# Kernel optimization log

Hardware: AMD Instinct MI355X
Metric: run time of the kernel (lower is better)

Reference implementation:

```python
import jax, jax.numpy as jnp
import numpy as np

B, S, D, H, FF = 4, 1024, 1024, 16, 4096
DH = D // H
EPS = 1e-5  # torch LayerNorm default


def _layernorm(x, g, b):
    m = jnp.mean(x, axis=-1, keepdims=True)
    v = jnp.mean((x - m) ** 2, axis=-1, keepdims=True)
    return (x - m) * jax.lax.rsqrt(v + EPS) * g + b


def setup_inputs() -> dict:
    key = jax.random.key(0)
    ks = jax.random.split(key, 8)
    init = lambda k, shape: jax.random.normal(k, shape, jnp.float32) * 0.02
    return {
        "x": jax.random.normal(ks[0], (B, S, D), jnp.float32),
        "Wq": init(ks[1], (D, D)), "bq": jnp.zeros((D,), jnp.float32),
        "Wk": init(ks[2], (D, D)), "bk": jnp.zeros((D,), jnp.float32),
        "Wv": init(ks[3], (D, D)), "bv": jnp.zeros((D,), jnp.float32),
        "Wo": init(ks[4], (D, D)), "bo": jnp.zeros((D,), jnp.float32),
        "ln1_g": jnp.ones((D,), jnp.float32), "ln1_b": jnp.zeros((D,), jnp.float32),
        "W1": init(ks[5], (D, FF)), "b1": jnp.zeros((FF,), jnp.float32),
        "W2": init(ks[6], (FF, D)), "b2": jnp.zeros((D,), jnp.float32),
        "ln2_g": jnp.ones((D,), jnp.float32), "ln2_b": jnp.zeros((D,), jnp.float32),
    }


def reference(x, Wq, bq, Wk, bk, Wv, bv, Wo, bo,
              ln1_g, ln1_b, W1, b1, W2, b2, ln2_g, ln2_b):
    Bx, Sx, _ = x.shape

    def heads(w, b):  # [B,S,D] -> [B,H,S,DH]
        return (x @ w + b).reshape(Bx, Sx, H, DH).transpose(0, 2, 1, 3)

    q, k, v = heads(Wq, bq), heads(Wk, bk), heads(Wv, bv)
    scores = jnp.einsum('bhqd,bhkd->bhqk', q, k) / jnp.sqrt(jnp.float32(DH))
    causal = jnp.tril(jnp.ones((Sx, Sx), bool))
    scores = jnp.where(causal[None, None], scores, jnp.float32(-1e9))
    attn = jax.nn.softmax(scores, axis=-1)           # [B,H,S,S]
    ctx = jnp.einsum('bhqk,bhkd->bqhd', attn, v).reshape(Bx, Sx, D)
    attn_out = ctx @ Wo + bo
    h = _layernorm(x + attn_out, ln1_g, ln1_b)
    ff = jax.nn.relu(h @ W1 + b1) @ W2 + b2
    y = _layernorm(h + ff, ln2_g, ln2_b)
    return (y, attn)
```

## Files before the change

kernel.cpp:

```cpp
#include <hip/hip_runtime.h>
#include <cstdint>


#define T_B 4
#define T_S 1024
#define T_D 1024
#define T_H 16
#define T_DH 64
#define T_FF 4096
#define T_TOK (T_B * T_S)

typedef __attribute__((ext_vector_type(8))) short bf16x8;
typedef __attribute__((ext_vector_type(4))) float f32x4;

__device__ __forceinline__ short f2bf(float f) {
  uint32_t u = __float_as_uint(f);
  u += 0x7FFFu + ((u >> 16) & 1u);
  return (short)(u >> 16);
}

__device__ __forceinline__ float bf2f(short s) {
  return __uint_as_float(((uint32_t)(unsigned short)s) << 16);
}

__device__ __forceinline__ void async_copy16(void* lds, const void* g) {
  __builtin_amdgcn_global_load_lds(
      (__attribute__((address_space(1))) uint32_t*)(uintptr_t)g,
      (__attribute__((address_space(3))) uint32_t*)(uint32_t)(uintptr_t)lds,
      16, 0, 0);
}

__device__ __forceinline__ void stage32(short* dstA, short* dstB,
                                        const short* A, int lda, const short* Bm,
                                        int ldb, int m0, int n0, int k0, int t,
                                        int wid) {
  const int row0 = t >> 2;
  const int cb0 = (t & 3) << 4;
  async_copy16((char*)dstA + (wid << 10),
               (const char*)A + (((size_t)(m0 + row0) * lda + k0) << 1) + cb0);
  async_copy16((char*)dstA + 4096 + (wid << 10),
               (const char*)A + (((size_t)(m0 + 64 + row0) * lda + k0) << 1) + cb0);
  async_copy16((char*)dstB + (wid << 10),
               (const char*)Bm + (((size_t)(n0 + row0) * ldb + k0) << 1) + cb0);
  async_copy16((char*)dstB + 4096 + (wid << 10),
               (const char*)Bm + (((size_t)(n0 + 64 + row0) * ldb + k0) << 1) + cb0);
}

__device__ __forceinline__ void compute32(const short* As, const short* Bs,
                                          int wm, int wn, int quad, int r16,
                                          f32x4 acc[4][4]) {
  bf16x8 av[4], bv[4];
#pragma unroll
  for (int i = 0; i < 4; ++i) {
    av[i] = *(const bf16x8*)(As + ((wm + i * 16 + r16) << 5) + (quad << 3));
    bv[i] = *(const bf16x8*)(Bs + ((wn + i * 16 + r16) << 5) + (quad << 3));
  }
#pragma unroll
  for (int mi = 0; mi < 4; ++mi)
#pragma unroll
    for (int ni = 0; ni < 4; ++ni)
      acc[mi][ni] = __builtin_amdgcn_mfma_f32_16x16x32_bf16(av[mi], bv[ni],
                                                            acc[mi][ni], 0, 0, 0);
}

__device__ __forceinline__ void mfma_loop_bk64(
    const short* __restrict__ A, int lda, const short* __restrict__ Bm, int ldb,
    int kLen, int m0, int n0, short* As, short* As2, short* Bs, short* Bs2,
    f32x4 acc[4][4]) {
  const int t = threadIdx.x;
  const int lane = t & 63, wid = t >> 6;
  const int wm = (wid >> 1) << 6, wn = (wid & 1) << 6;
  const int quad = lane >> 4, r16 = lane & 15;
  const f32x4 zf = {0.f, 0.f, 0.f, 0.f};
#pragma unroll
  for (int i = 0; i < 4; ++i)
#pragma unroll
    for (int j = 0; j < 4; ++j) acc[i][j] = zf;
  for (int k0 = 0; k0 < kLen; k0 += 64) {
    __syncthreads();
    stage32(As, Bs, A, lda, Bm, ldb, m0, n0, k0, t, wid);
    stage32(As2, Bs2, A, lda, Bm, ldb, m0, n0, k0 + 32, t, wid);
    __syncthreads();
    compute32(As, Bs, wm, wn, quad, r16, acc);
    compute32(As2, Bs2, wm, wn, quad, r16, acc);
  }
}

template <int MODE>
__global__ __launch_bounds__(256) void gemm_dense(
    const short* __restrict__ A, const short* __restrict__ Bw, int K, int N,
    const float* __restrict__ bias0, const float* __restrict__ bias1,
    const float* __restrict__ bias2, short* __restrict__ outb0,
    short* __restrict__ outb1, short* __restrict__ outb2) {
  __shared__ __align__(16) char smem[MODE == 0 ? 34816 : 32768];
  short* As = (short*)smem;
  short* As2 = As + 4096;
  short* Bs = As + 8192;
  short* Bs2 = As + 12288;
  const int m0 = blockIdx.x << 7, n0 = blockIdx.y << 7;
  f32x4 acc[4][4];
  mfma_loop_bk64(A, K, Bw, K, K, m0, n0, As, As2, Bs, Bs2, acc);

  const int t = threadIdx.x;
  const int lane = t & 63, wid = t >> 6;
  const int wm = (wid >> 1) << 6, wn = (wid & 1) << 6;
  const int quad = lane >> 4, r16 = lane & 15;

  if constexpr (MODE == 0) {
    const int which = n0 >> 10;
    const float* bias = (which == 0) ? bias0 : (which == 1) ? bias1 : bias2;
    if (which < 2) {
      short* outp = (which == 0) ? outb0 : outb1;
#pragma unroll
      for (int mi = 0; mi < 4; ++mi) {
#pragma unroll
        for (int ni = 0; ni < 4; ++ni) {
          const int col = n0 + wn + ni * 16 + r16;
          const int c10 = col & 1023;
          const float bb = bias[c10];
          const int hh = c10 >> 6, dh = col & 63;
#pragma unroll
          for (int reg = 0; reg < 4; ++reg) {
            const int row = m0 + wm + mi * 16 + quad * 4 + reg;
            const int b = row >> 10, s = row & 1023;
            outp[((((size_t)b * T_H + hh) * T_S) + s) * T_DH + dh] =
                f2bf(acc[mi][ni][reg] + bb);
          }
        }
      }
    } else {
      __syncthreads();
      short* vtile = (short*)smem;
#pragma unroll
      for (int mi = 0; mi < 4; ++mi)
#pragma unroll
        for (int ni = 0; ni < 4; ++ni) {
          const int c = wn + ni * 16 + r16;
          const float bb = bias[(n0 + c) & 1023];
#pragma unroll
          for (int reg = 0; reg < 4; ++reg) {
            const int r = wm + mi * 16 + quad * 4 + reg;
            vtile[c * 136 + r] = f2bf(acc[mi][ni][reg] + bb);
          }
        }
      __syncthreads();
      const int b = m0 >> 10, s0 = m0 & 1023;
      const int c = t >> 1, half = t & 1;
      const int c10 = (n0 + c) & 1023;
      const int hh = c10 >> 6, dh = c10 & 63;
      short* dst = outb2 + (((size_t)b * T_H + hh) * T_DH + dh) * T_S + s0 + half * 64;
      const short* srcl = vtile + c * 136 + half * 64;
#pragma unroll
      for (int j = 0; j < 8; ++j)
        *(bf16x8*)(dst + j * 8) = *(const bf16x8*)(srcl + j * 8);
    }
  } else {
#pragma unroll
    for (int mi = 0; mi < 4; ++mi)
#pragma unroll
      for (int ni = 0; ni < 4; ++ni) {
        const int col = n0 + wn + ni * 16 + r16;
        const float bb = bias0[col];
#pragma unroll
        for (int reg = 0; reg < 4; ++reg) {
          const int row = m0 + wm + mi * 16 + quad * 4 + reg;
          outb0[(size_t)row * N + col] = f2bf(fmaxf(acc[mi][ni][reg] + bb, 0.f));
        }
      }
  }
}

__global__ __launch_bounds__(256) void gemm_splitk(
    const short* __restrict__ A, const short* __restrict__ Bw, int K, int N,
    int kc, float* __restrict__ outp) {
  __shared__ __align__(16) char smem[32768];
  short* As = (short*)smem;
  short* As2 = As + 4096;
  short* Bs = As + 8192;
  short* Bs2 = As + 12288;
  const int m0 = blockIdx.x << 7, n0 = blockIdx.y << 7, z = blockIdx.z;
  f32x4 acc[4][4];
  mfma_loop_bk64(A + (size_t)z * kc, K, Bw + (size_t)z * kc, K, kc, m0, n0, As,
                 As2, Bs, Bs2, acc);
  float* o = outp + (size_t)z * T_TOK * N;
  const int t = threadIdx.x;
  const int lane = t & 63, wid = t >> 6;
  const int wm = (wid >> 1) << 6, wn = (wid & 1) << 6;
  const int quad = lane >> 4, r16 = lane & 15;
#pragma unroll
  for (int mi = 0; mi < 4; ++mi)
#pragma unroll
    for (int ni = 0; ni < 4; ++ni) {
      const int col = n0 + wn + ni * 16 + r16;
#pragma unroll
      for (int reg = 0; reg < 4; ++reg) {
        const int row = m0 + wm + mi * 16 + quad * 4 + reg;
        o[(size_t)row * N + col] = acc[mi][ni][reg];
      }
    }
}

__global__ __launch_bounds__(256) void attn_pass1(
    const short* __restrict__ qg, const short* __restrict__ kg,
    const short* __restrict__ vg, short* __restrict__ ctx,
    float* __restrict__ rsinv_g) {
  const int qb = blockIdx.x;
  const int bh = blockIdx.y;
  const int b = bh >> 4, h = bh & 15;
  const int m0 = qb << 7;
  __shared__ __align__(16) short Es[4 * 128 * 32];
  __shared__ float rsbuf[2][128];
  const int t = threadIdx.x;
  const int lane = t & 63, wid = t >> 6;
  const int quad = lane >> 4, r16 = lane & 15;
  const int wm = (wid >> 1) << 6, wn = (wid & 1) << 6;
  const int pvm = wid << 5;

  const short* Qbh = qg + (size_t)bh * T_S * T_DH;
  const short* Kbh = kg + (size_t)bh * T_S * T_DH;
  const short* Vbh = vg + (size_t)bh * T_DH * T_S;

  bf16x8 qf[4][2];
#pragma unroll
  for (int mi = 0; mi < 4; ++mi)
#pragma unroll
    for (int ksd = 0; ksd < 2; ++ksd)
      qf[mi][ksd] = *(const bf16x8*)(Qbh + (size_t)(m0 + wm + mi * 16 + r16) * T_DH +
                                     ksd * 32 + quad * 8);

  float rs[4][4];
#pragma unroll
  for (int i = 0; i < 4; ++i)
#pragma unroll
    for (int j = 0; j < 4; ++j) rs[i][j] = 0.f;
  const f32x4 zf = {0.f, 0.f, 0.f, 0.f};
  f32x4 accp[2][4];
#pragma unroll
  for (int i = 0; i < 2; ++i)
#pragma unroll
    for (int j = 0; j < 4; ++j) accp[i][j] = zf;

  for (int kt = 0; kt <= qb; ++kt) {
    f32x4 accs[4][4];
#pragma unroll
    for (int i = 0; i < 4; ++i)
#pragma unroll
      for (int j = 0; j < 4; ++j) accs[i][j] = zf;
#pragma unroll
    for (int ksd = 0; ksd < 2; ++ksd) {
      bf16x8 bv[4];
#pragma unroll
      for (int ni = 0; ni < 4; ++ni)
        bv[ni] = *(const bf16x8*)(Kbh + (size_t)(kt * 128 + wn + ni * 16 + r16) * T_DH +
                                  ksd * 32 + quad * 8);
#pragma unroll
      for (int mi = 0; mi < 4; ++mi)
#pragma unroll
        for (int ni = 0; ni < 4; ++ni)
          accs[mi][ni] = __builtin_amdgcn_mfma_f32_16x16x32_bf16(
              qf[mi][ksd], bv[ni], accs[mi][ni], 0, 0, 0);
    }
    __syncthreads();
    const bool diag = (kt == qb);
#pragma unroll
    for (int mi = 0; mi < 4; ++mi) {
#pragma unroll
      for (int ni = 0; ni < 4; ++ni) {
        const int cbase = wn + ni * 16;
        const int kse = cbase >> 5;
        const int sin = (cbase & 31) + r16;
        short* ep = Es + kse * 4096 + (wm + mi * 16 + quad * 4) * 32 + sin;
        const int colw = cbase + r16;
#pragma unroll
        for (int reg = 0; reg < 4; ++reg) {
          float e = __expf(accs[mi][ni][reg] * 0.125f);
          if (diag && colw > (wm + mi * 16 + quad * 4 + reg)) e = 0.f;
          ep[reg * 32] = f2bf(e);
          rs[mi][reg] += e;
        }
      }
    }
    __syncthreads();
#pragma unroll
    for (int ks = 0; ks < 4; ++ks) {
      bf16x8 av[2], bvv[4];
#pragma unroll
      for (int i = 0; i < 2; ++i)
        av[i] = *(const bf16x8*)(Es + ks * 4096 + (pvm + i * 16 + r16) * 32 + quad * 8);
#pragma unroll
      for (int ni = 0; ni < 4; ++ni)
        bvv[ni] = *(const bf16x8*)(Vbh + (size_t)(ni * 16 + r16) * T_S + kt * 128 +
                                   ks * 32 + quad * 8);
#pragma unroll
      for (int i = 0; i < 2; ++i)
#pragma unroll
        for (int ni = 0; ni < 4; ++ni)
          accp[i][ni] = __builtin_amdgcn_mfma_f32_16x16x32_bf16(av[i], bvv[ni],
                                                                accp[i][ni], 0, 0, 0);
    }
  }

#pragma unroll
  for (int mi = 0; mi < 4; ++mi)
#pragma unroll
    for (int reg = 0; reg < 4; ++reg) {
#pragma unroll
      for (int d = 1; d < 16; d <<= 1)
        rs[mi][reg] += __shfl_xor(rs[mi][reg], d, 64);
    }
  if (r16 == 0) {
#pragma unroll
    for (int mi = 0; mi < 4; ++mi)
#pragma unroll
      for (int reg = 0; reg < 4; ++reg)
        rsbuf[wid & 1][wm + mi * 16 + quad * 4 + reg] = rs[mi][reg];
  }
  __syncthreads();
  if (t < 128) {
    const float iv = 1.f / (rsbuf[0][t] + rsbuf[1][t]);
    rsbuf[0][t] = iv;
    rsinv_g[(size_t)bh * T_S + m0 + t] = iv;
  }
  __syncthreads();
#pragma unroll
  for (int i = 0; i < 2; ++i)
#pragma unroll
    for (int ni = 0; ni < 4; ++ni) {
#pragma unroll
      for (int reg = 0; reg < 4; ++reg) {
        const int row = pvm + i * 16 + quad * 4 + reg;
        const float iv = rsbuf[0][row];
        ctx[((size_t)b * T_S + m0 + row) * T_D + h * 64 + ni * 16 + r16] =
            f2bf(accp[i][ni][reg] * iv);
      }
    }
}

__global__ __launch_bounds__(256) void attn_pass2(
    const short* __restrict__ qg, const short* __restrict__ kg,
    const float* __restrict__ rsinv_g, float* __restrict__ attn) {
  const int qb = blockIdx.x, kt = blockIdx.y, bh = blockIdx.z;
  float* out = attn + ((size_t)bh * T_S + qb * 128) * T_S + kt * 128;
  const int t = threadIdx.x;
  if (kt > qb) {
    const float4 z4 = {0.f, 0.f, 0.f, 0.f};
#pragma unroll
    for (int j = 0; j < 16; ++j) {
      const int id = t + j * 256;
      ((float4*)(out + (size_t)(id >> 5) * T_S))[id & 31] = z4;
    }
    return;
  }
  const int lane = t & 63, wid = t >> 6;
  const int quad = lane >> 4, r16 = lane & 15;
  const int wm = (wid >> 1) << 6, wn = (wid & 1) << 6;
  const short* Qbh = qg + (size_t)bh * T_S * T_DH;
  const short* Kbh = kg + (size_t)bh * T_S * T_DH;
  const f32x4 zf = {0.f, 0.f, 0.f, 0.f};
  f32x4 accs[4][4];
#pragma unroll
  for (int i = 0; i < 4; ++i)
#pragma unroll
    for (int j = 0; j < 4; ++j) accs[i][j] = zf;
#pragma unroll
  for (int ksd = 0; ksd < 2; ++ksd) {
    bf16x8 aq[4], bv[4];
#pragma unroll
    for (int mi = 0; mi < 4; ++mi)
      aq[mi] = *(const bf16x8*)(Qbh + (size_t)(qb * 128 + wm + mi * 16 + r16) * T_DH +
                                ksd * 32 + quad * 8);
#pragma unroll
    for (int ni = 0; ni < 4; ++ni)
      bv[ni] = *(const bf16x8*)(Kbh + (size_t)(kt * 128 + wn + ni * 16 + r16) * T_DH +
                                ksd * 32 + quad * 8);
#pragma unroll
    for (int mi = 0; mi < 4; ++mi)
#pragma unroll
      for (int ni = 0; ni < 4; ++ni)
        accs[mi][ni] = __builtin_amdgcn_mfma_f32_16x16x32_bf16(aq[mi], bv[ni],
                                                               accs[mi][ni], 0, 0, 0);
  }
  const bool diag = (kt == qb);
#pragma unroll
  for (int mi = 0; mi < 4; ++mi)
#pragma unroll
    for (int ni = 0; ni < 4; ++ni) {
      const int col = wn + ni * 16 + r16;
#pragma unroll
      for (int reg = 0; reg < 4; ++reg) {
        const int rowt = wm + mi * 16 + quad * 4 + reg;
        const float iv = rsinv_g[(size_t)bh * T_S + qb * 128 + rowt];
        float e = __expf(accs[mi][ni][reg] * 0.125f) * iv;
        if (diag && col > rowt) e = 0.f;
        out[(size_t)rowt * T_S + col] = e;
      }
    }
}

__global__ __launch_bounds__(256) void ln_multi(
    const float* __restrict__ a32, const short* __restrict__ a16,
    const float* __restrict__ parts, int nparts, const float* __restrict__ bias,
    const float* __restrict__ g, const float* __restrict__ be,
    float* __restrict__ outf, short* __restrict__ outb) {
  const int row = blockIdx.x;
  const int t = threadIdx.x;
  float4 x;
  if (a32 != nullptr) {
    x = ((const float4*)(a32 + (size_t)row * T_D))[t];
  } else {
    const short4 s4 = ((const short4*)(a16 + (size_t)row * T_D))[t];
    x.x = bf2f(s4.x); x.y = bf2f(s4.y); x.z = bf2f(s4.z); x.w = bf2f(s4.w);
  }
  const float4 bv = ((const float4*)bias)[t];
  x.x += bv.x; x.y += bv.y; x.z += bv.z; x.w += bv.w;
  for (int p = 0; p < nparts; ++p) {
    const float4 v =
        ((const float4*)(parts + (size_t)p * T_TOK * T_D + (size_t)row * T_D))[t];
    x.x += v.x; x.y += v.y; x.z += v.z; x.w += v.w;
  }
  float sum = x.x + x.y + x.z + x.w;
  float sq = x.x * x.x + x.y * x.y + x.z * x.z + x.w * x.w;
  __shared__ float reds[4], redq[4];
  const int lane = t & 63, wid = t >> 6;
#pragma unroll
  for (int o = 32; o > 0; o >>= 1) {
    sum += __shfl_down(sum, o, 64);
    sq += __shfl_down(sq, o, 64);
  }
  if (lane == 0) { reds[wid] = sum; redq[wid] = sq; }
  __syncthreads();
  sum = reds[0] + reds[1] + reds[2] + reds[3];
  sq = redq[0] + redq[1] + redq[2] + redq[3];
  const float mean = sum * (1.f / T_D);
  const float var = sq * (1.f / T_D) - mean * mean;
  const float rstd = rsqrtf(var + 1e-5f);
  const float4 gg = ((const float4*)g)[t];
  const float4 bb = ((const float4*)be)[t];
  float4 y;
  y.x = (x.x - mean) * rstd * gg.x + bb.x;
  y.y = (x.y - mean) * rstd * gg.y + bb.y;
  y.z = (x.z - mean) * rstd * gg.z + bb.z;
  y.w = (x.w - mean) * rstd * gg.w + bb.w;
  if (outf != nullptr) ((float4*)(outf + (size_t)row * T_D))[t] = y;
  if (outb != nullptr) {
    short4 o4;
    o4.x = f2bf(y.x); o4.y = f2bf(y.y); o4.z = f2bf(y.z); o4.w = f2bf(y.w);
    ((short4*)(outb + (size_t)row * T_D))[t] = o4;
  }
}

__global__ __launch_bounds__(256) void prep_kernel(
    const float* __restrict__ x, short* __restrict__ xb,
    const float* __restrict__ Wq, const float* __restrict__ Wk,
    const float* __restrict__ Wv, const float* __restrict__ Wo,
    const float* __restrict__ W1, const float* __restrict__ W2,
    short* __restrict__ Wqkv_t, short* __restrict__ Wo_t,
    short* __restrict__ W1_t, short* __restrict__ W2_t) {
  int id = blockIdx.x;
  const int t = threadIdx.x;
  if (id < 4096) {
    const int i = id * 256 + t;
    const float4 v = ((const float4*)x)[i];
    short4 o;
    o.x = f2bf(v.x); o.y = f2bf(v.y); o.z = f2bf(v.z); o.w = f2bf(v.w);
    ((short4*)xb)[i] = o;
    return;
  }
  id -= 4096;
  const float* src;
  short* dst;
  int R, C;
  if (id < 1024) { src = Wq; dst = Wqkv_t; R = 1024; C = 1024; }
  else if (id < 2048) { id -= 1024; src = Wk; dst = Wqkv_t + 1024 * 1024; R = 1024; C = 1024; }
  else if (id < 3072) { id -= 2048; src = Wv; dst = Wqkv_t + 2 * 1024 * 1024; R = 1024; C = 1024; }
  else if (id < 4096) { id -= 3072; src = Wo; dst = Wo_t; R = 1024; C = 1024; }
  else if (id < 8192) { id -= 4096; src = W1; dst = W1_t; R = 1024; C = 4096; }
  else { id -= 8192; src = W2; dst = W2_t; R = 4096; C = 1024; }
  const int tilesC = C >> 5;
  const int r0 = (id / tilesC) << 5, c0 = (id % tilesC) << 5;
  __shared__ float tile[32][33];
  const int tx = t & 31, ty = t >> 5;
#pragma unroll
  for (int j = 0; j < 4; ++j)
    tile[ty + j * 8][tx] = src[(size_t)(r0 + ty + j * 8) * C + c0 + tx];
  __syncthreads();
#pragma unroll
  for (int j = 0; j < 4; ++j)
    dst[(size_t)(c0 + ty + j * 8) * R + r0 + tx] = f2bf(tile[tx][ty + j * 8]);
}

extern "C" void kernel_launch(void* const* d_in, const int* in_sizes, int n_in,
                              void* d_out, int out_size, void* d_ws,
                              size_t ws_size, hipStream_t stream) {
  const float* x = (const float*)d_in[0];
  const float* Wq = (const float*)d_in[1];
  const float* bq = (const float*)d_in[2];
  const float* Wk = (const float*)d_in[3];
  const float* bk = (const float*)d_in[4];
  const float* Wv = (const float*)d_in[5];
  const float* bv = (const float*)d_in[6];
  const float* Wo = (const float*)d_in[7];
  const float* bo = (const float*)d_in[8];
  const float* ln1g = (const float*)d_in[9];
  const float* ln1b = (const float*)d_in[10];
  const float* W1 = (const float*)d_in[11];
  const float* b1 = (const float*)d_in[12];
  const float* W2 = (const float*)d_in[13];
  const float* b2 = (const float*)d_in[14];
  const float* ln2g = (const float*)d_in[15];
  const float* ln2b = (const float*)d_in[16];
  (void)in_sizes; (void)n_in; (void)out_size; (void)ws_size;

  float* y_out = (float*)d_out;
  float* attn = (float*)d_out + (size_t)T_TOK * T_D;

  char* w = (char*)d_ws;
  size_t off = 0;
  auto alloc = [&](size_t bytes) -> void* {
    void* p = w + off;
    off += (bytes + 255) & ~(size_t)255;
    return p;
  };
  short* xb     = (short*)alloc((size_t)T_TOK * T_D * 2);
  short* Wqkv_t = (short*)alloc((size_t)3 * T_D * T_D * 2);
  short* Wo_t   = (short*)alloc((size_t)T_D * T_D * 2);
  short* W1_t   = (short*)alloc((size_t)T_FF * T_D * 2);
  short* W2_t   = (short*)alloc((size_t)T_D * T_FF * 2);
  short* qb_    = (short*)alloc((size_t)T_TOK * T_D * 2);
  short* kb_    = (short*)alloc((size_t)T_TOK * T_D * 2);
  short* vtb    = (short*)alloc((size_t)T_TOK * T_D * 2);
  short* ctx    = (short*)alloc((size_t)T_TOK * T_D * 2);
  short* hb     = (short*)alloc((size_t)T_TOK * T_D * 2);
  short* ff1    = (short*)alloc((size_t)T_TOK * T_FF * 2);
  float* rsinv  = (float*)alloc((size_t)T_H * T_B * T_S * 4);
  float* woP    = (float*)alloc((size_t)2 * T_TOK * T_D * 4);
  float* ffP    = (float*)alloc((size_t)2 * T_TOK * T_D * 4);

  prep_kernel<<<dim3(16384), dim3(256), 0, stream>>>(
      x, xb, Wq, Wk, Wv, Wo, W1, W2, Wqkv_t, Wo_t, W1_t, W2_t);

  gemm_dense<0><<<dim3(32, 24), dim3(256), 0, stream>>>(
      xb, Wqkv_t, T_D, 3072, bq, bk, bv, qb_, kb_, vtb);
  attn_pass1<<<dim3(8, 64), dim3(256), 0, stream>>>(qb_, kb_, vtb, ctx, rsinv);
  attn_pass2<<<dim3(8, 8, 64), dim3(256), 0, stream>>>(qb_, kb_, rsinv, attn);

  gemm_splitk<<<dim3(32, 8, 2), dim3(256), 0, stream>>>(ctx, Wo_t, T_D, T_D, 512, woP);
  ln_multi<<<dim3(4096), dim3(256), 0, stream>>>(x, nullptr, woP, 2, bo, ln1g,
                                                 ln1b, nullptr, hb);

  gemm_dense<2><<<dim3(32, 32), dim3(256), 0, stream>>>(
      hb, W1_t, T_D, T_FF, b1, nullptr, nullptr, ff1, nullptr, nullptr);
  gemm_splitk<<<dim3(32, 8, 2), dim3(256), 0, stream>>>(ff1, W2_t, T_FF, T_D, 2048, ffP);
  ln_multi<<<dim3(4096), dim3(256), 0, stream>>>(nullptr, hb, ffP, 2, b2, ln2g,
                                                 ln2b, y_out, nullptr);
}
```

Before: 637.6 us.

## Replace synchronous GEMM k-loop with three-stage async LDS ring pipeline

Rewrites the shared GEMM main loop so that global-to-LDS async copies for k-step it+2 are issued while step it computes. A three-slot LDS ring, synchronised with vmcnt waits and a single barrier per 32-wide k step, replaces the earlier load-all, sync, compute pattern. The aim is to hide global load latency behind MFMA work. In exchange, LDS per block grows to 48KB, which may reduce occupancy. The MODE 0 epilogue previously had 34816 bytes of LDS, so it may depend on the smem layout.

```diff
diff --git a/kernel.cpp b/kernel.cpp
--- a/kernel.cpp
+++ b/kernel.cpp
@@ -30,20 +30,13 @@
       16, 0, 0);
 }
 
-__device__ __forceinline__ void stage32(short* dstA, short* dstB,
-                                        const short* A, int lda, const short* Bm,
-                                        int ldb, int m0, int n0, int k0, int t,
-                                        int wid) {
-  const int row0 = t >> 2;
-  const int cb0 = (t & 3) << 4;
-  async_copy16((char*)dstA + (wid << 10),
-               (const char*)A + (((size_t)(m0 + row0) * lda + k0) << 1) + cb0);
-  async_copy16((char*)dstA + 4096 + (wid << 10),
-               (const char*)A + (((size_t)(m0 + 64 + row0) * lda + k0) << 1) + cb0);
-  async_copy16((char*)dstB + (wid << 10),
-               (const char*)Bm + (((size_t)(n0 + row0) * ldb + k0) << 1) + cb0);
-  async_copy16((char*)dstB + 4096 + (wid << 10),
-               (const char*)Bm + (((size_t)(n0 + 64 + row0) * ldb + k0) << 1) + cb0);
+__device__ __forceinline__ void stage_ring(char* base, const char* gA0,
+                                           const char* gA1, const char* gB0,
+                                           const char* gB1, int koffB, int wid) {
+  async_copy16(base + (wid << 10), gA0 + koffB);
+  async_copy16(base + 4096 + (wid << 10), gA1 + koffB);
+  async_copy16(base + 8192 + (wid << 10), gB0 + koffB);
+  async_copy16(base + 12288 + (wid << 10), gB1 + koffB);
 }
 
 __device__ __forceinline__ void compute32(const short* As, const short* Bs,
@@ -63,26 +56,51 @@
                                                             acc[mi][ni], 0, 0, 0);
 }
 
-__device__ __forceinline__ void mfma_loop_bk64(
+__device__ __forceinline__ void mfma_loop_ring(
     const short* __restrict__ A, int lda, const short* __restrict__ Bm, int ldb,
-    int kLen, int m0, int n0, short* As, short* As2, short* Bs, short* Bs2,
-    f32x4 acc[4][4]) {
+    int kLen, int m0, int n0, char* smem, f32x4 acc[4][4]) {
   const int t = threadIdx.x;
   const int lane = t & 63, wid = t >> 6;
   const int wm = (wid >> 1) << 6, wn = (wid & 1) << 6;
   const int quad = lane >> 4, r16 = lane & 15;
+  const int row0 = t >> 2, cb0 = (t & 3) << 4;
+  const char* gA0 = (const char*)A + (((size_t)(m0 + row0) * lda) << 1) + cb0;
+  const char* gA1 = gA0 + ((size_t)lda << 7);
+  const char* gB0 = (const char*)Bm + (((size_t)(n0 + row0) * ldb) << 1) + cb0;
+  const char* gB1 = gB0 + ((size_t)ldb << 7);
+
   const f32x4 zf = {0.f, 0.f, 0.f, 0.f};
 #pragma unroll
   for (int i = 0; i < 4; ++i)
 #pragma unroll
     for (int j = 0; j < 4; ++j) acc[i][j] = zf;
-  for (int k0 = 0; k0 < kLen; k0 += 64) {
-    __syncthreads();
-    stage32(As, Bs, A, lda, Bm, ldb, m0, n0, k0, t, wid);
-    stage32(As2, Bs2, A, lda, Bm, ldb, m0, n0, k0 + 32, t, wid);
-    __syncthreads();
+
+  const int nIter = kLen >> 5;
+  stage_ring(smem, gA0, gA1, gB0, gB1, 0, wid);
+  stage_ring(smem + 16384, gA0, gA1, gB0, gB1, 64, wid);
+  asm volatile("s_waitcnt vmcnt(4)" ::: "memory");
+  __builtin_amdgcn_s_barrier();
+  __builtin_amdgcn_sched_barrier(0);
+
+  int cur = 0;
+  for (int it = 0; it < nIter; ++it) {
+    const int k2 = (it + 2) << 5;
+    if (k2 < kLen) {
+      int nb = cur + 2;
+      if (nb >= 3) nb -= 3;
+      stage_ring(smem + nb * 16384, gA0, gA1, gB0, gB1, k2 << 1, wid);
+    }
+    const short* As = (const short*)(smem + cur * 16384);
+    const short* Bs = (const short*)(smem + cur * 16384 + 8192);
     compute32(As, Bs, wm, wn, quad, r16, acc);
-    compute32(As2, Bs2, wm, wn, quad, r16, acc);
+    if (k2 < kLen)
+      asm volatile("s_waitcnt vmcnt(4)" ::: "memory");
+    else
+      asm volatile("s_waitcnt vmcnt(0)" ::: "memory");
+    __builtin_amdgcn_s_barrier();
+    __builtin_amdgcn_sched_barrier(0);
+    ++cur;
+    if (cur >= 3) cur -= 3;
   }
 }
 
@@ -92,14 +110,10 @@
     const float* __restrict__ bias0, const float* __restrict__ bias1,
     const float* __restrict__ bias2, short* __restrict__ outb0,
     short* __restrict__ outb1, short* __restrict__ outb2) {
-  __shared__ __align__(16) char smem[MODE == 0 ? 34816 : 32768];
-  short* As = (short*)smem;
-  short* As2 = As + 4096;
-  short* Bs = As + 8192;
-  short* Bs2 = As + 12288;
+  __shared__ __align__(16) char smem[49152];
   const int m0 = blockIdx.x << 7, n0 = blockIdx.y << 7;
   f32x4 acc[4][4];
-  mfma_loop_bk64(A, K, Bw, K, K, m0, n0, As, As2, Bs, Bs2, acc);
+  mfma_loop_ring(A, K, Bw, K, K, m0, n0, smem, acc);
 
   const int t = threadIdx.x;
   const int lane = t & 63, wid = t >> 6;
@@ -173,15 +187,11 @@
 __global__ __launch_bounds__(256) void gemm_splitk(
     const short* __restrict__ A, const short* __restrict__ Bw, int K, int N,
     int kc, float* __restrict__ outp) {
-  __shared__ __align__(16) char smem[32768];
-  short* As = (short*)smem;
-  short* As2 = As + 4096;
-  short* Bs = As + 8192;
-  short* Bs2 = As + 12288;
+  __shared__ __align__(16) char smem[49152];
   const int m0 = blockIdx.x << 7, n0 = blockIdx.y << 7, z = blockIdx.z;
   f32x4 acc[4][4];
-  mfma_loop_bk64(A + (size_t)z * kc, K, Bw + (size_t)z * kc, K, kc, m0, n0, As,
-                 As2, Bs, Bs2, acc);
+  mfma_loop_ring(A + (size_t)z * kc, K, Bw + (size_t)z * kc, K, kc, m0, n0,
+                 smem, acc);
   float* o = outp + (size_t)z * T_TOK * N;
   const int t = threadIdx.x;
   const int lane = t & 63, wid = t >> 6;
```

New measurement: 623.1 us. -2.3%, faster.
